# Performance work log

Hardware: AMD Instinct MI355X
Metric: run time of the kernel (lower is better)

The kernel has to match this reference:

```python
import jax, jax.numpy as jnp
import numpy as np
import math

B, TQ, TK = 64, 1024, 512
CONV_CH, EMBED_DIM, ATT_HID = 512, 512, 512
KEY_POS_RATE = 1.385
QUERY_POS_RATE = 1.0
POSITION_WEIGHT = 1.0


def sin_pos_enc(positions, w, d):
    # positions: [B, T] int, padding_idx=0 maps to zero vector.
    # pe[..., 2i]   = sin(w*pos / 10000^(2i/d))
    # pe[..., 2i+1] = cos(w*pos / 10000^(2i/d))
    i = jnp.arange(d)
    inv_freq = jnp.power(jnp.float32(10000.0), -(2.0 * (i // 2).astype(jnp.float32)) / d)  # [d]
    ang = (positions.astype(jnp.float32) * w)[..., None] * inv_freq  # [B, T, d]
    pe = jnp.where(i % 2 == 0, jnp.sin(ang), jnp.cos(ang))
    return jnp.where((positions == 0)[..., None], jnp.float32(0.0), pe)


def setup_inputs() -> dict:
    key = jax.random.key(0)
    ks = jax.random.split(key, 12)
    s = 0.02
    inp = {
        "query": jax.random.normal(ks[0], (B, TQ, CONV_CH), jnp.float32),
        "keys": jax.random.normal(ks[1], (B, TK, EMBED_DIM), jnp.float32),
        "values": jax.random.normal(ks[2], (B, TK, EMBED_DIM), jnp.float32),
        # 1-based positions (0 is the padding index of SinusoidalEncoding)
        "text_positions": jnp.broadcast_to(jnp.arange(1, TK + 1, dtype=jnp.int64), (B, TK)),
        "frame_positions": jnp.broadcast_to(jnp.arange(1, TQ + 1, dtype=jnp.int64), (B, TQ)),
        # pad mask over keys: last 64 text positions are padding
        "mask": jnp.broadcast_to(jnp.arange(TK) >= (TK - 64), (B, TK)),
        "Wq": jax.random.normal(ks[3], (CONV_CH, ATT_HID), jnp.float32) * s,
        "bq": jnp.zeros((ATT_HID,), jnp.float32),
        "Wk": jax.random.normal(ks[4], (EMBED_DIM, ATT_HID), jnp.float32) * s,
        "bk": jnp.zeros((ATT_HID,), jnp.float32),
        "Wv": jax.random.normal(ks[5], (EMBED_DIM, ATT_HID), jnp.float32) * s,
        "bv": jnp.zeros((ATT_HID,), jnp.float32),
        "Wo": jax.random.normal(ks[6], (ATT_HID, CONV_CH), jnp.float32) * s,
        "bo": jnp.zeros((CONV_CH,), jnp.float32),
    }
    return inp


def reference(query, keys, values, text_positions, frame_positions, mask,
              Wq, bq, Wk, bk, Wv, bv, Wo, bo):
    # positional-bias injection (position_weight = 1.0)
    keys = keys + POSITION_WEIGHT * sin_pos_enc(text_positions, KEY_POS_RATE, EMBED_DIM)[:, :keys.shape[1], :]
    query = query + POSITION_WEIGHT * sin_pos_enc(frame_positions, QUERY_POS_RATE, CONV_CH)[:, :frame_positions.shape[-1], :]

    v = values @ Wv + bv            # [B, TK, H]
    k = keys @ Wk + bk              # [B, TK, H]
    q = query @ Wq + bq             # [B, TQ, H]

    scores = jnp.einsum('bqh,bkh->bqk', q, k)               # [B, TQ, TK]
    scores = jnp.where(mask[:, None, :], -jnp.inf, scores)
    attn = jax.nn.softmax(scores, axis=2)
    # dropout is a no-op in eval mode
    x = jnp.einsum('bqk,bkh->bqh', attn, v)
    x = x * jnp.float32(math.sqrt(1.0 / v.shape[1]))
    out = x @ Wo + bo               # [B, TQ, conv_channels]
    return out, attn
```

## Files before the change

kernel.cpp:

```cpp
#include <hip/hip_runtime.h>
#include <stdint.h>

#define DEVI __device__ __forceinline__

typedef __attribute__((ext_vector_type(4))) float     f4v;
typedef __attribute__((ext_vector_type(8))) _Float16  h8;
typedef __attribute__((ext_vector_type(4))) _Float16  h4;
typedef unsigned int  u32;

static constexpr int   TQ = 1024, TKN = 512;
static constexpr float KEY_RATE = 1.385f;
static constexpr float QRY_RATE = 1.0f;
static constexpr float SCALE    = 0.04419417382415922f;
static constexpr float INVC     = 0.05190512648261504f;

static constexpr size_t OFF_MM   = 0;
static constexpr size_t OFF_NT   = OFF_MM  + (size_t)512*512*2;
static constexpr size_t OFF_WOT  = OFF_NT  + (size_t)512*512*2;
static constexpr size_t OFF_PEQ  = OFF_WOT + (size_t)512*512*4;
static constexpr size_t OFF_W    = OFF_PEQ + (size_t)1024*512*4;
static constexpr size_t OFF_C    = OFF_W   + 512*4;
static constexpr size_t OFF_BQBK = OFF_C   + 512*4;
static constexpr size_t OFF_T    = OFF_BQBK + 256;
static constexpr size_t OFF_KP   = OFF_T   + (size_t)64*512*4;
static constexpr size_t OFF_MKT  = OFF_KP  + (size_t)64*512*512*2;
static constexpr size_t OFF_PT   = OFF_MKT + (size_t)64*512*512*2;
static constexpr size_t WS_NEED  = OFF_PT  + (size_t)64*512*512*2;
static constexpr size_t OFF_A16  = WS_NEED;
static constexpr size_t WS_BIG   = OFF_A16 + (size_t)64*1024*512*2;

#define WAITV(N) asm volatile("s_waitcnt vmcnt(" #N ")" ::: "memory")
#define WAITL()  asm volatile("s_waitcnt lgkmcnt(0)" ::: "memory")
#define SCHEDB() __builtin_amdgcn_sched_barrier(0)
#define BARRAW() __builtin_amdgcn_s_barrier()

DEVI f4v mfma16(h8 a, h8 b, f4v c) {
  return __builtin_amdgcn_mfma_f32_16x16x32_f16(a, b, c, 0, 0, 0);
}

DEVI void gld16(void* lds, const void* g) {
  __builtin_amdgcn_global_load_lds(
      (const __attribute__((address_space(1))) unsigned int*)g,
      (__attribute__((address_space(3))) unsigned int*)lds, 16, 0, 0);
}

DEVI void stage_B(char* Bbuf, const _Float16* B, int k0, int tid) {
#pragma unroll
  for (int it = 0; it < 4; ++it) {
    const int c = (it << 9) + tid;
    const int r = c >> 2, s = c & 3;
    const int sg = s ^ ((r >> 1) & 3);
    gld16(Bbuf + ((size_t)c << 4), B + (size_t)r * 512 + k0 + (sg << 3));
  }
}

DEVI void stage_A16(char* Abuf, const _Float16* A, int k0, int tid) {
  const int r = tid >> 2, s = tid & 3;
  const int sg = s ^ ((r >> 1) & 3);
  gld16(Abuf + ((size_t)tid << 4), A + (size_t)r * 512 + k0 + (sg << 3));
}

DEVI void loads_A32(f4v& x0, f4v& x1, const float* A, const float* add, int k0, int tid) {
  const int r = tid >> 2, c8 = (tid & 3) << 3;
  const float* p = A + (size_t)r * 512 + k0 + c8;
  x0 = *(const f4v*)p; x1 = *(const f4v*)(p + 4);
  if (add) {
    const float* q = add + (size_t)r * 512 + k0 + c8;
    x0 += *(const f4v*)q; x1 += *(const f4v*)(q + 4);
  }
}
DEVI void write_A32(char* Abuf, f4v x0, f4v x1, int tid) {
  const int r = tid >> 2;
  const int slot = (tid & 3) ^ ((r >> 1) & 3);
  h8 o;
#pragma unroll
  for (int i = 0; i < 4; ++i) { o[i] = (_Float16)x0[i]; o[4 + i] = (_Float16)x1[i]; }
  *(h8*)(Abuf + (r << 6) + (slot << 4)) = o;
}

DEVI void read_fragsA(const char* Ab, int wr, int lane, h8 (&a)[4]) {
  const int l15 = lane & 15, hi = lane >> 4;
#pragma unroll
  for (int mi = 0; mi < 4; ++mi) {
    const int r = wr * 64 + mi * 16 + l15;
    a[mi] = *(const h8*)(Ab + (r << 6) + ((hi ^ ((r >> 1) & 3)) << 4));
  }
}
DEVI void read_fragsB(const char* Bb, int wc, int lane, h8 (&b)[8]) {
  const int l15 = lane & 15, hi = lane >> 4;
#pragma unroll
  for (int nj = 0; nj < 8; ++nj) {
    const int g = wc * 128 + nj * 16 + l15;
    b[nj] = *(const h8*)(Bb + (g << 6) + ((hi ^ ((g >> 1) & 3)) << 4));
  }
}

#define MFMA_ALL(a, bf, acc)                                   \
  _Pragma("unroll") for (int mi = 0; mi < 4; ++mi)             \
  _Pragma("unroll") for (int nj = 0; nj < 8; ++nj)             \
      acc[mi][nj] = mfma16(a[mi], bf[nj], acc[mi][nj]);

#define REG_PIPELINE(As, Ad, Bs, acc)                                              \
  {                                                                                \
    char* const Abf[2] = {lds, lds + 8192};                                        \
    char* const Bbf[3] = {lds + 16384, lds + 49152, lds + 81920};                  \
    f4v x0, x1;                                                                    \
    loads_A32(x0, x1, As, Ad, 0, tid);                                             \
    SCHEDB();                                                                      \
    stage_B(Bbf[0], Bs, 0, tid);                                                   \
    stage_B(Bbf[1], Bs, 32, tid);                                                  \
    write_A32(Abf[0], x0, x1, tid);                                                \
    WAITV(4); WAITL(); SCHEDB(); BARRAW(); SCHEDB();                               \
    _Pragma("unroll")                                                              \
    for (int k = 0; k < 16; ++k) {                                                 \
      if (k < 15) { loads_A32(x0, x1, As, Ad, (k + 1) * 32, tid); SCHEDB(); }      \
      if (k < 14) stage_B(Bbf[(k + 2) % 3], Bs, (k + 2) * 32, tid);                \
      h8 a[4], bf[8];                                                              \
      read_fragsA(Abf[k & 1], wr, lane, a);                                        \
      read_fragsB(Bbf[k % 3], wc, lane, bf);                                       \
      MFMA_ALL(a, bf, acc);                                                        \
      if (k < 15) write_A32(Abf[(k + 1) & 1], x0, x1, tid);                        \
      if (k < 14) { WAITV(4); } else if (k == 14) { WAITV(0); }                    \
      if (k < 15) { WAITL(); SCHEDB(); BARRAW(); SCHEDB(); }                       \
    }                                                                              \
  }

#define GLD_PIPELINE(As, Bs, acc)                                                  \
  {                                                                                \
    char* const Abf[3] = {lds, lds + 8192, lds + 16384};                           \
    char* const Bbf[3] = {lds + 24576, lds + 57344, lds + 90112};                  \
    stage_A16(Abf[0], As, 0, tid);  stage_B(Bbf[0], Bs, 0, tid);                   \
    stage_A16(Abf[1], As, 32, tid); stage_B(Bbf[1], Bs, 32, tid);                  \
    WAITV(5); SCHEDB(); BARRAW(); SCHEDB();                                        \
    _Pragma("unroll")                                                              \
    for (int k = 0; k < 16; ++k) {                                                 \
      if (k < 14) {                                                                \
        stage_A16(Abf[(k + 2) % 3], As, (k + 2) * 32, tid);                        \
        stage_B(Bbf[(k + 2) % 3], Bs, (k + 2) * 32, tid);                          \
      }                                                                            \
      h8 a[4], bf[8];                                                              \
      read_fragsA(Abf[k % 3], wr, lane, a);                                        \
      read_fragsB(Bbf[k % 3], wc, lane, bf);                                       \
      MFMA_ALL(a, bf, acc);                                                        \
      if (k < 14) { WAITV(5); } else if (k == 14) { WAITV(0); }                    \
      if (k < 15) { WAITL(); SCHEDB(); BARRAW(); SCHEDB(); }                       \
    }                                                                              \
  }

DEVI void stage_f32_A(char* Abuf, const float* A, int k0, int tid) {
#pragma unroll
  for (int it = 0; it < 2; ++it) {
    const int idx = (it << 9) + tid;
    const int r = idx >> 3, c4 = idx & 7;
    f4v x = *(const f4v*)(A + (size_t)r * 512 + k0 + (c4 << 2));
    h4 o;
#pragma unroll
    for (int i = 0; i < 4; ++i) o[i] = (_Float16)x[i];
    const int slot = (c4 >> 1) ^ ((r >> 1) & 3);
    *(h4*)(Abuf + (r << 6) + (slot << 4) + ((c4 & 1) << 3)) = o;
  }
}
DEVI void stage_f32_B(char* Bbuf, const float* B, int k0, int tid) {
#pragma unroll
  for (int it = 0; it < 8; ++it) {
    const int idx = (it << 9) + tid;
    const int r = idx >> 3, c4 = idx & 7;
    f4v x = *(const f4v*)(B + (size_t)r * 512 + k0 + (c4 << 2));
    h4 o;
#pragma unroll
    for (int i = 0; i < 4; ++i) o[i] = (_Float16)x[i];
    const int slot = (c4 >> 1) ^ ((r >> 1) & 3);
    *(h4*)(Bbuf + (r << 6) + (slot << 4) + ((c4 & 1) << 3)) = o;
  }
}

__global__ __launch_bounds__(256) void k_prepA(
    const float* __restrict__ Wk, const float* __restrict__ bq,
    const float* __restrict__ bk, const float* __restrict__ bv,
    const float* __restrict__ Wo, const float* __restrict__ bo,
    const void* __restrict__ fpos_raw,
    float* __restrict__ wvec, float* __restrict__ cvec, float* __restrict__ bqbk,
    float* __restrict__ PEQ, float* __restrict__ WoT) {
  const int bid = blockIdx.x, tid = threadIdx.x;
  if (bid < 128) {
    const int wid = tid >> 6, lane = tid & 63;
    const int row = bid * 4 + wid;
    const float* p = Wk + (size_t)row * 512 + lane * 8;
    const f4v a = *(const f4v*)p, c = *(const f4v*)(p + 4);
    const f4v b0 = *(const f4v*)(bq + lane * 8), b1 = *(const f4v*)(bq + lane * 8 + 4);
    float d = a[0]*b0[0]+a[1]*b0[1]+a[2]*b0[2]+a[3]*b0[3]
            + c[0]*b1[0]+c[1]*b1[1]+c[2]*b1[2]+c[3]*b1[3];
#pragma unroll
    for (int off = 32; off; off >>= 1) d += __shfl_xor(d, off);
    if (lane == 0) wvec[row] = d;
  } else if (bid == 128) {
    __shared__ float red[256];
#pragma unroll
    for (int u = 0; u < 2; ++u) {
      const int i = tid + u * 256;
      float acc = 0.f;
      for (int a = 0; a < 512; ++a) acc += bv[a] * Wo[(size_t)a * 512 + i];
      cvec[i] = SCALE * acc + bo[i];
    }
    red[tid] = bq[tid] * bk[tid] + bq[tid + 256] * bk[tid + 256];
    __syncthreads();
    if (tid == 0) { float s = 0.f; for (int h = 0; h < 256; ++h) s += red[h]; bqbk[0] = s; }
  } else if (bid < 129 + 2048) {
    const u32* fp = (const u32*)fpos_raw;
    const bool is64 = (fp[1] == 0);
    const int t = (bid - 129) * 256 + tid;
    const int tq = t >> 9, d = t & 511;
    const int pos = (int)(is64 ? fp[2 * tq] : fp[tq]);
    float pe = 0.f;
    if (pos != 0) {
      const float invf = exp2f(-(float)(d >> 1) * INVC);
      const float ang  = ((float)pos * QRY_RATE) * invf;
      pe = (d & 1) ? cosf(ang) : sinf(ang);
    }
    PEQ[t] = pe;
  } else {
    __shared__ float t[32][33];
    const int local = bid - 2177;
    const int bx = local & 15, by = local >> 4;
    const int tx = tid & 31, ty = tid >> 5;
    const int x = bx * 32 + tx;
#pragma unroll
    for (int j = 0; j < 4; ++j)
      t[ty + 8 * j][tx] = Wo[(size_t)(by * 32 + ty + 8 * j) * 512 + x];
    __syncthreads();
    const int x2 = by * 32 + tx;
#pragma unroll
    for (int j = 0; j < 4; ++j)
      WoT[(size_t)(bx * 32 + ty + 8 * j) * 512 + x2] = t[tx][ty + 8 * j];
  }
}

__global__ __launch_bounds__(512) void k_prepB(
    const float* __restrict__ Wq, const float* __restrict__ Wk,
    const float* __restrict__ WoT, const float* __restrict__ Wv,
    const float* __restrict__ keys, const void* __restrict__ tpos_raw,
    const void* __restrict__ mask_raw,
    const float* __restrict__ wvec, const float* __restrict__ bqbk,
    _Float16* __restrict__ Mm, _Float16* __restrict__ Nt,
    _Float16* __restrict__ kp, float* __restrict__ tvec) {
  __shared__ char lds[40960];
  const int bid = blockIdx.x, tid = threadIdx.x;
  const int lane = tid & 63, wid = tid >> 6;
  if (bid < 8) {
    char *Ab = lds, *Bb = lds + 8192;
    const int wr = wid >> 2, wc = wid & 3;
    const int x = bid & 3, y = bid >> 2;
    const float* A = (y == 0 ? Wq : WoT) + (size_t)x * 128 * 512;
    const float* B = (y == 0 ? Wk : Wv);
    _Float16* out = (y == 0 ? Mm : Nt) + (size_t)x * 128 * 512;
    f4v acc[4][8] = {};
    for (int ks = 0; ks < 16; ++ks) {
      stage_f32_A(Ab, A, ks * 32, tid);
      stage_f32_B(Bb, B, ks * 32, tid);
      __syncthreads();
      h8 a[4], bf[8];
      read_fragsA(Ab, wr, lane, a);
      read_fragsB(Bb, wc, lane, bf);
      MFMA_ALL(a, bf, acc);
      __syncthreads();
    }
    const int l15 = lane & 15, hi = lane >> 4;
#pragma unroll
    for (int mi = 0; mi < 4; ++mi)
#pragma unroll
      for (int nj = 0; nj < 8; ++nj) {
        const int col = wc * 128 + nj * 16 + l15;
#pragma unroll
        for (int j = 0; j < 4; ++j) {
          const int row = wr * 64 + mi * 16 + hi * 4 + j;
          out[(size_t)row * 512 + col] = (_Float16)acc[mi][nj][j];
        }
      }
  } else {
    const u32* tp = (const u32*)tpos_raw;
    const bool is64 = (tp[1] == 0);
    const int row = (bid - 8) * 8 + wid;
    const int pos = (int)(is64 ? tp[2 * row] : tp[row]);
    const int d0  = lane * 8;
    const float* src = keys + (size_t)row * 512 + d0;
    const f4v a = *(const f4v*)src, b = *(const f4v*)(src + 4);
    float x[8] = {a[0], a[1], a[2], a[3], b[0], b[1], b[2], b[3]};
    if (pos != 0) {
      const float pw = (float)pos * KEY_RATE;
#pragma unroll
      for (int u = 0; u < 4; ++u) {
        const float invf = exp2f(-(float)(lane * 4 + u) * INVC);
        const float ang  = pw * invf;
        x[2*u]   += sinf(ang);
        x[2*u+1] += cosf(ang);
      }
    }
    const f4v w0 = *(const f4v*)(wvec + d0), w1 = *(const f4v*)(wvec + d0 + 4);
    float dot = 0.f;
#pragma unroll
    for (int i = 0; i < 4; ++i) dot += x[i] * w0[i] + x[4+i] * w1[i];
#pragma unroll
    for (int off = 32; off; off >>= 1) dot += __shfl_xor(dot, off);
    if (lane == 0) {
      const u32* m32 = (const u32*)mask_raw;
      const bool is32 = (m32[448] != 0);
      const bool mk = is32 ? (m32[row] != 0)
                           : (((const unsigned char*)mask_raw)[row] != 0);
      tvec[row] = mk ? -1e30f : (dot + bqbk[0]);
    }
    h8 o;
#pragma unroll
    for (int i = 0; i < 8; ++i) o[i] = (_Float16)x[i];
    *(h8*)(kp + (size_t)row * 512 + d0) = o;
  }
}

__global__ __launch_bounds__(512, 1) void k_mkpv(
    const _Float16* __restrict__ kp, const _Float16* __restrict__ Mm,
    const float* __restrict__ values, const _Float16* __restrict__ Nt,
    _Float16* __restrict__ MKt, _Float16* __restrict__ Pt) {
  __shared__ char lds[122880];
  const int bid = blockIdx.x, tid = threadIdx.x;
  const int lane = tid & 63, wid = tid >> 6;
  const int wr = wid >> 2, wc = wid & 3;
  const int l15 = lane & 15, hi = lane >> 4;
  f4v acc[4][8] = {};
  if (bid < 256) {
    const int tt = bid & 3, b = bid >> 2;
    const _Float16* As = kp + ((size_t)b * TKN + tt * 128) * 512;
    GLD_PIPELINE(As, Mm, acc);
    _Float16* Ob = MKt + (size_t)b * TKN * 512 + (size_t)tt * 128 * 512;
#pragma unroll
    for (int mi = 0; mi < 4; ++mi)
#pragma unroll
      for (int nj = 0; nj < 8; ++nj) {
        const int col = wc * 128 + nj * 16 + l15;
#pragma unroll
        for (int j = 0; j < 4; ++j) {
          const int row = wr * 64 + mi * 16 + hi * 4 + j;
          Ob[(size_t)row * 512 + col] = (_Float16)acc[mi][nj][j];
        }
      }
  } else {
    const int rt = (bid - 256) & 3, b = (bid - 256) >> 2;
    const float* As = values + ((size_t)b * TKN + rt * 128) * 512;
    const float* Ad = nullptr;
    REG_PIPELINE(As, Ad, Nt, acc);
    _Float16* Pb = Pt + (size_t)b * 512 * 512;
#pragma unroll
    for (int mi = 0; mi < 4; ++mi)
#pragma unroll
      for (int nj = 0; nj < 8; ++nj) {
        const int col = wc * 128 + nj * 16 + l15;
        const int t0  = rt * 128 + wr * 64 + mi * 16 + hi * 4;
        h4 o;
#pragma unroll
        for (int j = 0; j < 4; ++j) o[j] = (_Float16)acc[mi][nj][j];
        *(h4*)(Pb + (size_t)col * 512 + t0) = o;
      }
  }
}

__global__ __launch_bounds__(512, 1) void k_scores(
    const float* __restrict__ query, const float* __restrict__ PEQ,
    const _Float16* __restrict__ MKt, const float* __restrict__ tve,
    float* __restrict__ attn, _Float16* __restrict__ a16) {
  __shared__ char lds[114688];
  const int tid = threadIdx.x, lane = tid & 63, wid = tid >> 6;
  const int wr = wid >> 2, wc = wid & 3;
  const int qt = blockIdx.x, b = blockIdx.y;
  const float* As = query + ((size_t)b * TQ + qt * 128) * 512;
  const float* Ad = PEQ + (size_t)(qt * 128) * 512;
  const _Float16* Bs = MKt + (size_t)b * TKN * 512;
  const int l15 = lane & 15, hi = lane >> 4;
  float tv[8];
#pragma unroll
  for (int nj = 0; nj < 8; ++nj) tv[nj] = tve[b * TKN + wc * 128 + nj * 16 + l15];
  f4v acc[4][8] = {};
  REG_PIPELINE(As, Ad, Bs, acc);
  float* red  = (float*)lds;
  float* red2 = (float*)(lds + 2048);
#pragma unroll
  for (int mi = 0; mi < 4; ++mi)
#pragma unroll
    for (int nj = 0; nj < 8; ++nj) {
      const float t = tv[nj];
#pragma unroll
      for (int j = 0; j < 4; ++j) acc[mi][nj][j] += t;
    }
  float mrow[4][4];
#pragma unroll
  for (int mi = 0; mi < 4; ++mi)
#pragma unroll
    for (int j = 0; j < 4; ++j) {
      float m = acc[mi][0][j];
#pragma unroll
      for (int nj = 1; nj < 8; ++nj) m = fmaxf(m, acc[mi][nj][j]);
      m = fmaxf(m, __shfl_xor(m, 1)); m = fmaxf(m, __shfl_xor(m, 2));
      m = fmaxf(m, __shfl_xor(m, 4)); m = fmaxf(m, __shfl_xor(m, 8));
      mrow[mi][j] = m;
    }
  __syncthreads();
  if (l15 == 0) {
#pragma unroll
    for (int mi = 0; mi < 4; ++mi)
#pragma unroll
      for (int j = 0; j < 4; ++j)
        red[(wr * 64 + mi * 16 + hi * 4 + j) * 4 + wc] = mrow[mi][j];
  }
  __syncthreads();
#pragma unroll
  for (int mi = 0; mi < 4; ++mi)
#pragma unroll
    for (int j = 0; j < 4; ++j) {
      const f4v rv = *(const f4v*)(red + (wr * 64 + mi * 16 + hi * 4 + j) * 4);
      mrow[mi][j] = fmaxf(fmaxf(rv[0], rv[1]), fmaxf(rv[2], rv[3]));
    }
  float srow[4][4];
#pragma unroll
  for (int mi = 0; mi < 4; ++mi)
#pragma unroll
    for (int j = 0; j < 4; ++j) {
      float s = 0.f;
      const float m = mrow[mi][j];
#pragma unroll
      for (int nj = 0; nj < 8; ++nj) {
        const float e = expf(acc[mi][nj][j] - m);
        acc[mi][nj][j] = e; s += e;
      }
      s += __shfl_xor(s, 1); s += __shfl_xor(s, 2);
      s += __shfl_xor(s, 4); s += __shfl_xor(s, 8);
      srow[mi][j] = s;
    }
  if (l15 == 0) {
#pragma unroll
    for (int mi = 0; mi < 4; ++mi)
#pragma unroll
      for (int j = 0; j < 4; ++j)
        red2[(wr * 64 + mi * 16 + hi * 4 + j) * 4 + wc] = srow[mi][j];
  }
  __syncthreads();
  float* Ao = attn + ((size_t)b * TQ + qt * 128) * 512;
  _Float16* Ah = a16 ? a16 + ((size_t)b * TQ + qt * 128) * 512 : nullptr;
#pragma unroll
  for (int mi = 0; mi < 4; ++mi)
#pragma unroll
    for (int j = 0; j < 4; ++j) {
      const int row = wr * 64 + mi * 16 + hi * 4 + j;
      const f4v sv = *(const f4v*)(red2 + row * 4);
      const float rinv = 1.f / (sv[0] + sv[1] + sv[2] + sv[3]);
#pragma unroll
      for (int nj = 0; nj < 8; ++nj) {
        const float v = acc[mi][nj][j] * rinv;
        const int col = wc * 128 + nj * 16 + l15;
        Ao[(size_t)row * 512 + col] = v;
        if (Ah) Ah[(size_t)row * 512 + col] = (_Float16)v;
      }
    }
}

template <int A16P>
__global__ __launch_bounds__(512, 1) void k_final(
    const float* __restrict__ attn, const _Float16* __restrict__ attn16,
    const _Float16* __restrict__ Pt, const float* __restrict__ cvec,
    float* __restrict__ outp) {
  __shared__ char lds[122880];
  const int tid = threadIdx.x, lane = tid & 63, wid = tid >> 6;
  const int wr = wid >> 2, wc = wid & 3;
  const int qt = blockIdx.x, b = blockIdx.y;
  const _Float16* Bs = Pt + (size_t)b * 512 * 512;
  const int l15 = lane & 15, hi = lane >> 4;
  f4v acc[4][8] = {};
  if (A16P) {
    const _Float16* As = attn16 + ((size_t)b * TQ + qt * 128) * 512;
    GLD_PIPELINE(As, Bs, acc);
  } else {
    const float* As = attn + ((size_t)b * TQ + qt * 128) * 512;
    const float* Ad = nullptr;
    REG_PIPELINE(As, Ad, Bs, acc);
  }
  float cv[8];
#pragma unroll
  for (int nj = 0; nj < 8; ++nj) cv[nj] = cvec[wc * 128 + nj * 16 + l15];
  float* Ob = outp + ((size_t)b * TQ + qt * 128) * 512;
#pragma unroll
  for (int mi = 0; mi < 4; ++mi)
#pragma unroll
    for (int nj = 0; nj < 8; ++nj) {
      const int col = wc * 128 + nj * 16 + l15;
#pragma unroll
      for (int j = 0; j < 4; ++j) {
        const int row = wr * 64 + mi * 16 + hi * 4 + j;
        Ob[(size_t)row * 512 + col] = SCALE * acc[mi][nj][j] + cv[nj];
      }
    }
}

extern "C" void kernel_launch(void* const* d_in, const int* in_sizes, int n_in,
                              void* d_out, int out_size, void* d_ws, size_t ws_size,
                              hipStream_t stream) {
  (void)in_sizes; (void)n_in; (void)out_size;
  if (ws_size < WS_NEED) return;
  const bool big = (ws_size >= WS_BIG);

  const float* query  = (const float*)d_in[0];
  const float* keys   = (const float*)d_in[1];
  const float* values = (const float*)d_in[2];
  const void*  tpos   = d_in[3];
  const void*  fpos   = d_in[4];
  const void*  mask   = d_in[5];
  const float* Wq = (const float*)d_in[6];
  const float* bq = (const float*)d_in[7];
  const float* Wk = (const float*)d_in[8];
  const float* bk = (const float*)d_in[9];
  const float* Wv = (const float*)d_in[10];
  const float* bv = (const float*)d_in[11];
  const float* Wo = (const float*)d_in[12];
  const float* bo = (const float*)d_in[13];

  char* ws = (char*)d_ws;
  _Float16* Mm   = (_Float16*)(ws + OFF_MM);
  _Float16* Nt   = (_Float16*)(ws + OFF_NT);
  float*    WoT  = (float*)   (ws + OFF_WOT);
  float*    PEQ  = (float*)   (ws + OFF_PEQ);
  float*    wvec = (float*)   (ws + OFF_W);
  float*    cvec = (float*)   (ws + OFF_C);
  float*    bqbk = (float*)   (ws + OFF_BQBK);
  float*    tvec = (float*)   (ws + OFF_T);
  _Float16* kp   = (_Float16*)(ws + OFF_KP);
  _Float16* MKt  = (_Float16*)(ws + OFF_MKT);
  _Float16* Pt   = (_Float16*)(ws + OFF_PT);
  _Float16* a16  = big ? (_Float16*)(ws + OFF_A16) : nullptr;

  float* outp = (float*)d_out;
  float* attn = outp + (size_t)64 * TQ * 512;

  k_prepA<<<2433, 256, 0, stream>>>(Wk, bq, bk, bv, Wo, bo, fpos,
                                    wvec, cvec, bqbk, PEQ, WoT);
  k_prepB<<<4104, 512, 0, stream>>>(Wq, Wk, WoT, Wv, keys, tpos, mask,
                                    wvec, bqbk, Mm, Nt, kp, tvec);
  k_mkpv <<<512, 512, 0, stream>>>(kp, Mm, values, Nt, MKt, Pt);
  k_scores<<<dim3(8, 64), 512, 0, stream>>>(query, PEQ, MKt, tvec, attn, a16);
  if (big) k_final<1><<<dim3(8, 64), 512, 0, stream>>>(attn, a16, Pt, cvec, outp);
  else     k_final<0><<<dim3(8, 64), 512, 0, stream>>>(attn, a16, Pt, cvec, outp);
}
```

Measured before the change: 346.7 us.

## Deepen A-prefetch pipeline, parallelize cvec, remap blocks per XCD

The register pipeline for fp32 A tiles now keeps two tiles of global loads in flight using ping-pong registers, hiding more global-load latency at the cost of extra VGPRs. The serial single-block cvec computation (bv·Wo) moves into k_prepB as 64 extra blocks doing wave-parallel dot products over the transposed WoT, removing a long single-block tail in k_prepA. k_scores and k_final switch to a 1D grid remapped so that all q-tiles of a batch land on the same XCD, so the shared B operand hits that XCD's L2 more often.

```diff
diff --git a/kernel.cpp b/kernel.cpp
--- a/kernel.cpp
+++ b/kernel.cpp
@@ -104,24 +104,33 @@
   {                                                                                \
     char* const Abf[2] = {lds, lds + 8192};                                        \
     char* const Bbf[3] = {lds + 16384, lds + 49152, lds + 81920};                  \
-    f4v x0, x1;                                                                    \
-    loads_A32(x0, x1, As, Ad, 0, tid);                                             \
+    f4v xa0, xa1, xb0, xb1;                                                        \
+    loads_A32(xa0, xa1, As, Ad, 0, tid);                                           \
+    loads_A32(xb0, xb1, As, Ad, 32, tid);                                          \
     SCHEDB();                                                                      \
     stage_B(Bbf[0], Bs, 0, tid);                                                   \
     stage_B(Bbf[1], Bs, 32, tid);                                                  \
-    write_A32(Abf[0], x0, x1, tid);                                                \
-    WAITV(4); WAITL(); SCHEDB(); BARRAW(); SCHEDB();                               \
+    WAITV(4);                                                                      \
+    write_A32(Abf[0], xa0, xa1, tid);                                              \
+    WAITL(); SCHEDB(); BARRAW(); SCHEDB();                                         \
     _Pragma("unroll")                                                              \
     for (int k = 0; k < 16; ++k) {                                                 \
-      if (k < 15) { loads_A32(x0, x1, As, Ad, (k + 1) * 32, tid); SCHEDB(); }      \
-      if (k < 14) stage_B(Bbf[(k + 2) % 3], Bs, (k + 2) * 32, tid);                \
+      if (k < 14) {                                                                \
+        if ((k & 1) == 0) { loads_A32(xa0, xa1, As, Ad, (k + 2) * 32, tid); }      \
+        else              { loads_A32(xb0, xb1, As, Ad, (k + 2) * 32, tid); }      \
+        SCHEDB();                                                                  \
+        stage_B(Bbf[(k + 2) % 3], Bs, (k + 2) * 32, tid);                          \
+      }                                                                            \
       h8 a[4], bf[8];                                                              \
       read_fragsA(Abf[k & 1], wr, lane, a);                                        \
       read_fragsB(Bbf[k % 3], wc, lane, bf);                                       \
       MFMA_ALL(a, bf, acc);                                                        \
-      if (k < 15) write_A32(Abf[(k + 1) & 1], x0, x1, tid);                        \
-      if (k < 14) { WAITV(4); } else if (k == 14) { WAITV(0); }                    \
-      if (k < 15) { WAITL(); SCHEDB(); BARRAW(); SCHEDB(); }                       \
+      if (k < 15) {                                                                \
+        if (k < 14) { WAITV(6); } else { WAITV(0); }                               \
+        if ((k & 1) == 0) write_A32(Abf[1], xb0, xb1, tid);                        \
+        else              write_A32(Abf[0], xa0, xa1, tid);                        \
+        WAITL(); SCHEDB(); BARRAW(); SCHEDB();                                     \
+      }                                                                            \
     }                                                                              \
   }
 
@@ -176,10 +185,10 @@
 
 __global__ __launch_bounds__(256) void k_prepA(
     const float* __restrict__ Wk, const float* __restrict__ bq,
-    const float* __restrict__ bk, const float* __restrict__ bv,
-    const float* __restrict__ Wo, const float* __restrict__ bo,
+    const float* __restrict__ bk,
+    const float* __restrict__ Wo,
     const void* __restrict__ fpos_raw,
-    float* __restrict__ wvec, float* __restrict__ cvec, float* __restrict__ bqbk,
+    float* __restrict__ wvec, float* __restrict__ bqbk,
     float* __restrict__ PEQ, float* __restrict__ WoT) {
   const int bid = blockIdx.x, tid = threadIdx.x;
   if (bid < 128) {
@@ -195,13 +204,6 @@
     if (lane == 0) wvec[row] = d;
   } else if (bid == 128) {
     __shared__ float red[256];
-#pragma unroll
-    for (int u = 0; u < 2; ++u) {
-      const int i = tid + u * 256;
-      float acc = 0.f;
-      for (int a = 0; a < 512; ++a) acc += bv[a] * Wo[(size_t)a * 512 + i];
-      cvec[i] = SCALE * acc + bo[i];
-    }
     red[tid] = bq[tid] * bk[tid] + bq[tid + 256] * bk[tid + 256];
     __syncthreads();
     if (tid == 0) { float s = 0.f; for (int h = 0; h < 256; ++h) s += red[h]; bqbk[0] = s; }
@@ -241,8 +243,10 @@
     const float* __restrict__ keys, const void* __restrict__ tpos_raw,
     const void* __restrict__ mask_raw,
     const float* __restrict__ wvec, const float* __restrict__ bqbk,
+    const float* __restrict__ bv, const float* __restrict__ bo,
     _Float16* __restrict__ Mm, _Float16* __restrict__ Nt,
-    _Float16* __restrict__ kp, float* __restrict__ tvec) {
+    _Float16* __restrict__ kp, float* __restrict__ tvec,
+    float* __restrict__ cvec) {
   __shared__ char lds[40960];
   const int bid = blockIdx.x, tid = threadIdx.x;
   const int lane = tid & 63, wid = tid >> 6;
@@ -276,7 +280,7 @@
           out[(size_t)row * 512 + col] = (_Float16)acc[mi][nj][j];
         }
       }
-  } else {
+  } else if (bid < 4104) {
     const u32* tp = (const u32*)tpos_raw;
     const bool is64 = (tp[1] == 0);
     const int row = (bid - 8) * 8 + wid;
@@ -312,6 +316,16 @@
 #pragma unroll
     for (int i = 0; i < 8; ++i) o[i] = (_Float16)x[i];
     *(h8*)(kp + (size_t)row * 512 + d0) = o;
+  } else {
+    const int row = (bid - 4104) * 8 + wid;
+    const float* p = WoT + (size_t)row * 512 + lane * 8;
+    const f4v a = *(const f4v*)p, c = *(const f4v*)(p + 4);
+    const f4v b0 = *(const f4v*)(bv + lane * 8), b1 = *(const f4v*)(bv + lane * 8 + 4);
+    float d = a[0]*b0[0]+a[1]*b0[1]+a[2]*b0[2]+a[3]*b0[3]
+            + c[0]*b1[0]+c[1]*b1[1]+c[2]*b1[2]+c[3]*b1[3];
+#pragma unroll
+    for (int off = 32; off; off >>= 1) d += __shfl_xor(d, off);
+    if (lane == 0) cvec[row] = SCALE * d + bo[row];
   }
 }
 
@@ -368,7 +382,9 @@
   __shared__ char lds[114688];
   const int tid = threadIdx.x, lane = tid & 63, wid = tid >> 6;
   const int wr = wid >> 2, wc = wid & 3;
-  const int qt = blockIdx.x, b = blockIdx.y;
+  const int bid = blockIdx.x;
+  const int xcd = bid & 7, i = bid >> 3;
+  const int qt = i & 7, b = xcd * 8 + (i >> 3);
   const float* As = query + ((size_t)b * TQ + qt * 128) * 512;
   const float* Ad = PEQ + (size_t)(qt * 128) * 512;
   const _Float16* Bs = MKt + (size_t)b * TKN * 512;
@@ -467,7 +483,9 @@
   __shared__ char lds[122880];
   const int tid = threadIdx.x, lane = tid & 63, wid = tid >> 6;
   const int wr = wid >> 2, wc = wid & 3;
-  const int qt = blockIdx.x, b = blockIdx.y;
+  const int bid = blockIdx.x;
+  const int xcd = bid & 7, i = bid >> 3;
+  const int qt = i & 7, b = xcd * 8 + (i >> 3);
   const _Float16* Bs = Pt + (size_t)b * 512 * 512;
   const int l15 = lane & 15, hi = lane >> 4;
   f4v acc[4][8] = {};
@@ -535,12 +553,11 @@
   float* outp = (float*)d_out;
   float* attn = outp + (size_t)64 * TQ * 512;
 
-  k_prepA<<<2433, 256, 0, stream>>>(Wk, bq, bk, bv, Wo, bo, fpos,
-                                    wvec, cvec, bqbk, PEQ, WoT);
-  k_prepB<<<4104, 512, 0, stream>>>(Wq, Wk, WoT, Wv, keys, tpos, mask,
-                                    wvec, bqbk, Mm, Nt, kp, tvec);
+  k_prepA<<<2433, 256, 0, stream>>>(Wk, bq, bk, Wo, fpos, wvec, bqbk, PEQ, WoT);
+  k_prepB<<<4168, 512, 0, stream>>>(Wq, Wk, WoT, Wv, keys, tpos, mask,
+                                    wvec, bqbk, bv, bo, Mm, Nt, kp, tvec, cvec);
   k_mkpv <<<512, 512, 0, stream>>>(kp, Mm, values, Nt, MKt, Pt);
-  k_scores<<<dim3(8, 64), 512, 0, stream>>>(query, PEQ, MKt, tvec, attn, a16);
-  if (big) k_final<1><<<dim3(8, 64), 512, 0, stream>>>(attn, a16, Pt, cvec, outp);
-  else     k_final<0><<<dim3(8, 64), 512, 0, stream>>>(attn, a16, Pt, cvec, outp);
-}
+  k_scores<<<512, 512, 0, stream>>>(query, PEQ, MKt, tvec, attn, a16);
+  if (big) k_final<1><<<512, 512, 0, stream>>>(attn, a16, Pt, cvec, outp);
+  else     k_final<0><<<512, 512, 0, stream>>>(attn, a16, Pt, cvec, outp);
+}
```

Measured after the change: 302.5 us. -12.8%, faster.
